# Performance work log

Measured on AMD Instinct MI355X. Metric: run time of the kernel, lower is better.

## Reference

```python
import jax, jax.numpy as jnp
import numpy as np

K = 3  # Chebyshev filter size (max_view)


def avwgcn(X, E, weights_pool, bias_pool):
    """Adaptive node-wise graph conv. X: [B,N,C_in], E: [N,D]."""
    N = E.shape[0]
    # adaptive adjacency: softmax over rows of relu(E E^T)
    supports = jax.nn.softmax(jax.nn.relu(E @ E.T), axis=1)  # [N,N]
    support_set = [jnp.eye(N, dtype=X.dtype), supports]
    for _ in range(2, K):  # Chebyshev recursion
        support_set.append(2.0 * supports @ support_set[-1] - support_set[-2])
    S = jnp.stack(support_set, axis=0)  # [K,N,N]
    W = jnp.einsum('nd,dkio->nkio', E, weights_pool)  # per-node weights [N,K,Ci,Co]
    bias = E @ bias_pool  # [N,Co]
    XG = jnp.einsum('knm,bmc->bnkc', S, X)  # [B,N,K,Ci]
    return jnp.einsum('bnki,nkio->bno', XG, W) + bias  # [B,N,Co]


def setup_inputs() -> dict:
    key = jax.random.key(0)
    ks = jax.random.split(key, 5)
    B, N, Cin, Cout, D = 32, 4096, 2, 64, 10
    Ci = Cin + Cout  # 66
    X = jax.random.normal(ks[0], (B, N, Cin), dtype=jnp.float32)
    H = jnp.zeros((B, N, Cout), dtype=jnp.float32)
    E = jax.random.normal(ks[1], (N, D), dtype=jnp.float32)
    W_gate = jax.random.normal(ks[2], (D, K, Ci, 2 * Cout), dtype=jnp.float32) * 0.1
    b_gate = jnp.zeros((D, 2 * Cout), dtype=jnp.float32)
    W_update = jax.random.normal(ks[3], (D, K, Ci, Cout), dtype=jnp.float32) * 0.1
    b_update = jnp.zeros((D, Cout), dtype=jnp.float32)
    return {"X": X, "H": H, "E": E, "W_gate": W_gate, "b_gate": b_gate,
            "W_update": W_update, "b_update": b_update}


def reference(X, H, E, W_gate, b_gate, W_update, b_update):
    Cout = H.shape[-1]
    XH = jnp.concatenate([X, H], axis=-1)  # [B,N,Cin+Cout]
    ZR = jax.nn.sigmoid(avwgcn(XH, E, W_gate, b_gate))  # [B,N,2*Cout]
    Z, R = ZR[..., :Cout], ZR[..., Cout:]
    C = jnp.concatenate([X, Z * H], axis=-1)
    HC = jnp.tanh(avwgcn(C, E, W_update, b_update))
    return R * H + (1.0 - R) * HC
```

## Files before the change

kernel.cpp:

```cpp
#include <hip/hip_runtime.h>
#include <math.h>

#define N_NODES 4096
#define BATCH   32
#define D_EMB   10
#define CIN     2
#define COUT    64
#define CI      66
#define KSUP    3
#define NCOLS   2112
#define NPAD    2176
#define LDT     4096

#define KSEC    72
#define KI_REAL 216
#define KILD    232
#define OCH     (32 * KILD)
#define WROW_G  (128 * KILD)
#define WROW_U  (64 * KILD)
#define WGT2_R  (WROW_G + WROW_U)

typedef _Float16 half_t;
typedef __attribute__((ext_vector_type(8))) _Float16 f16x8;
typedef __attribute__((ext_vector_type(4))) _Float16 f16x4;
typedef __attribute__((ext_vector_type(2))) _Float16 f16x2;
typedef __attribute__((ext_vector_type(4))) float f32x4;

union u32h2 { unsigned u; f16x2 h; };

struct __attribute__((packed, aligned(4))) uint4_u4 { uint4 v; };
__device__ __forceinline__ f16x8 loadu8h(const half_t* p) {
  union { uint4 u; f16x8 h; } r;
  r.u = ((const uint4_u4*)p)->v;
  return r.h;
}

__device__ __forceinline__ float fast_sigmoid(float x) { return 1.f / (1.f + __expf(-x)); }
__device__ __forceinline__ float fast_tanh(float x) { return 1.f - 2.f / (__expf(2.f * x) + 1.f); }

__device__ __forceinline__ void gld_lds16(const half_t* g, half_t* l) {
  __builtin_amdgcn_global_load_lds(
      (const __attribute__((address_space(1))) void*)g,
      (__attribute__((address_space(3))) void*)l, 16, 0, 0);
}

__global__ __launch_bounds__(256) void k_softmax_p(const float* __restrict__ E,
                                                   half_t* __restrict__ Pb) {
  const int n = blockIdx.x;
  const int tid = threadIdx.x;
  __shared__ float En[D_EMB];
  __shared__ float ms[256], ss[256];
  if (tid < D_EMB) En[tid] = E[n * D_EMB + tid];
  __syncthreads();
  float en[D_EMB];
#pragma unroll
  for (int d = 0; d < D_EMB; ++d) en[d] = En[d];

  float val[16];
  float m = -1e30f, s = 0.f;
#pragma unroll
  for (int it = 0; it < 16; ++it) {
    const int c = tid + it * 256;
    const float* Ec = E + c * D_EMB;
    float v = 0.f;
#pragma unroll
    for (int d = 0; d < D_EMB; ++d) v += en[d] * Ec[d];
    v = fmaxf(v, 0.f);
    val[it] = v;
    if (v > m) { s *= __expf(m - v); m = v; }
    s += __expf(v - m);
  }
  ms[tid] = m; ss[tid] = s;
  __syncthreads();
  for (int off = 128; off > 0; off >>= 1) {
    if (tid < off) {
      float m2 = ms[tid + off], s2 = ss[tid + off];
      float m1 = ms[tid], s1 = ss[tid];
      float mm = fmaxf(m1, m2);
      ms[tid] = mm;
      ss[tid] = s1 * __expf(m1 - mm) + s2 * __expf(m2 - mm);
    }
    __syncthreads();
  }
  const float M = ms[0];
  const float inv = 1.f / ss[0];
  half_t* Pr = Pb + (size_t)n * N_NODES;
#pragma unroll
  for (int it = 0; it < 16; ++it)
    Pr[tid + it * 256] = (half_t)(__expf(val[it] - M) * inv);
}

__global__ __launch_bounds__(256) void k_build_v0(const float* __restrict__ X,
                                                  const float* __restrict__ H,
                                                  half_t* __restrict__ Vt,
                                                  half_t* __restrict__ Vn,
                                                  half_t* __restrict__ Cbn) {
  size_t idx = (size_t)blockIdx.x * 256 + threadIdx.x;
  if (idx >= (size_t)N_NODES * NCOLS) return;
  const int m = (int)(idx / NCOLS);
  const int col = (int)(idx % NCOLS);
  const int b = col / CI;
  const int c = col % CI;
  float v;
  if (c < CIN) v = X[((size_t)b * N_NODES + m) * CIN + c];
  else         v = H[((size_t)b * N_NODES + m) * COUT + (c - CIN)];
  const half_t h = (half_t)v;
  Vn[(size_t)m * NPAD + col] = h;
  Vt[(size_t)col * LDT + m] = h;
  if (c < CIN) Cbn[(size_t)m * NPAD + col] = h;
}

__device__ __forceinline__ void gemm_compute_tile(const half_t* __restrict__ Lb,
                                                  int wm, int wn, int fofs,
                                                  f32x4 (&acc)[4][4]) {
  const half_t* As_ = Lb;
  const half_t* Bs_ = Lb + 4096;
  f16x8 a[4], b[4];
#pragma unroll
  for (int i = 0; i < 4; ++i)
    a[i] = *(const f16x8*)&As_[((wm >> 4) + i) * 512 + fofs];
#pragma unroll
  for (int j = 0; j < 4; ++j)
    b[j] = *(const f16x8*)&Bs_[((wn >> 4) + j) * 512 + fofs];
  __builtin_amdgcn_s_setprio(1);
#pragma unroll
  for (int i = 0; i < 4; ++i)
#pragma unroll
    for (int j = 0; j < 4; ++j)
      acc[i][j] = __builtin_amdgcn_mfma_f32_16x16x32_f16(a[i], b[j], acc[i][j], 0, 0, 0);
  __builtin_amdgcn_s_setprio(0);
}

__global__ __launch_bounds__(256) void k_gemm_f16(const half_t* __restrict__ A,
                                                  const half_t* __restrict__ Bt,
                                                  half_t* __restrict__ Cn,
                                                  half_t* __restrict__ Ct) {
  __shared__ half_t LB[4][8192];
  const int tid = threadIdx.x;
  const int lane = tid & 63;
  const int wave = tid >> 6;

  int flat = blockIdx.y * 17 + blockIdx.x;
  flat = (flat & 7) * 68 + (flat >> 3);
  const int bx = flat % 17;
  const int by = flat / 17;

  const int wm = (wave >> 1) * 64;
  const int wn = (wave & 1) * 64;
  const int rb = by * 128;
  const int cb = bx * 128;

  const int srow = lane >> 2;
  const int skg = (((lane & 3) + ((lane >> 3) & 3)) & 3) * 8;
  const half_t* ga0 = A + (size_t)(rb + wave * 32 + srow) * N_NODES + skg;
  const half_t* ga1 = ga0 + (size_t)16 * N_NODES;
  const half_t* gb0 = Bt + (size_t)(cb + wave * 32 + srow) * LDT + skg;
  const half_t* gb1 = gb0 + (size_t)16 * LDT;
  const int lA0 = wave * 1024;
  const int lA1 = lA0 + 512;
  const int lB0 = 4096 + wave * 1024;
  const int lB1 = lB0 + 512;

  const int fr = lane & 15;
  const int fg = lane >> 4;
  const int fofs = (4 * fr + ((fg - (fr >> 1)) & 3)) * 8;

  f32x4 acc[4][4] = {};

#define STAGE_T(buf, kk) do { half_t* Lp = LB[(buf)]; \
    gld_lds16(ga0 + (kk), Lp + lA0); gld_lds16(ga1 + (kk), Lp + lA1); \
    gld_lds16(gb0 + (kk), Lp + lB0); gld_lds16(gb1 + (kk), Lp + lB1); } while (0)

  STAGE_T(0, 0);
  STAGE_T(1, 32);
  STAGE_T(2, 64);

  for (int t = 0; t < 124; t += 4) {
    asm volatile("s_waitcnt vmcnt(8)\n\ts_barrier" ::: "memory");
    STAGE_T(3, (t + 3) * 32);
    gemm_compute_tile(LB[0], wm, wn, fofs, acc);

    asm volatile("s_waitcnt vmcnt(8)\n\ts_barrier" ::: "memory");
    STAGE_T(0, (t + 4) * 32);
    gemm_compute_tile(LB[1], wm, wn, fofs, acc);

    asm volatile("s_waitcnt vmcnt(8)\n\ts_barrier" ::: "memory");
    STAGE_T(1, (t + 5) * 32);
    gemm_compute_tile(LB[2], wm, wn, fofs, acc);

    asm volatile("s_waitcnt vmcnt(8)\n\ts_barrier" ::: "memory");
    STAGE_T(2, (t + 6) * 32);
    gemm_compute_tile(LB[3], wm, wn, fofs, acc);
  }
  asm volatile("s_waitcnt vmcnt(8)\n\ts_barrier" ::: "memory");
  STAGE_T(3, 127 * 32);
  gemm_compute_tile(LB[0], wm, wn, fofs, acc);
  asm volatile("s_waitcnt vmcnt(8)\n\ts_barrier" ::: "memory");
  gemm_compute_tile(LB[1], wm, wn, fofs, acc);
  asm volatile("s_waitcnt vmcnt(4)\n\ts_barrier" ::: "memory");
  gemm_compute_tile(LB[2], wm, wn, fofs, acc);
  asm volatile("s_waitcnt vmcnt(0)\n\ts_barrier" ::: "memory");
  gemm_compute_tile(LB[3], wm, wn, fofs, acc);
#undef STAGE_T

  const int en = lane & 15;
  const int em = (lane >> 4) * 4;
#pragma unroll
  for (int i = 0; i < 4; ++i) {
#pragma unroll
    for (int j = 0; j < 4; ++j) {
      const int m0 = rb + wm + i * 16 + em;
      const int n = cb + wn + j * 16 + en;
      half_t h0 = (half_t)acc[i][j][0];
      half_t h1 = (half_t)acc[i][j][1];
      half_t h2 = (half_t)acc[i][j][2];
      half_t h3 = (half_t)acc[i][j][3];
      if (Ct) {
        f16x4 t4 = {h0, h1, h2, h3};
        *(f16x4*)&Ct[(size_t)n * LDT + m0] = t4;
      }
      Cn[(size_t)(m0 + 0) * NPAD + n] = h0;
      Cn[(size_t)(m0 + 1) * NPAD + n] = h1;
      Cn[(size_t)(m0 + 2) * NPAD + n] = h2;
      Cn[(size_t)(m0 + 3) * NPAD + n] = h3;
    }
  }
}

__global__ __launch_bounds__(256) void k_tr(const half_t* __restrict__ Cbn,
                                            half_t* __restrict__ Ct) {
  __shared__ half_t T[64][69];
  const int tid = threadIdx.x;
  const int cb = blockIdx.x * 64;
  const int mb = blockIdx.y * 64;
  const int c4 = (tid & 15) * 4;
  const int r0 = tid >> 4;
#pragma unroll
  for (int it = 0; it < 4; ++it) {
    const int r = r0 + it * 16;
    f16x4 v = *(const f16x4*)&Cbn[(size_t)(mb + r) * NPAD + cb + c4];
    T[r][c4 + 0] = v[0];
    T[r][c4 + 1] = v[1];
    T[r][c4 + 2] = v[2];
    T[r][c4 + 3] = v[3];
  }
  __syncthreads();
#pragma unroll
  for (int it = 0; it < 4; ++it) {
    const int c2 = r0 + it * 16;
    const int m4 = c4;
    f16x4 v = {T[m4 + 0][c2], T[m4 + 1][c2], T[m4 + 2][c2], T[m4 + 3][c2]};
    *(f16x4*)&Ct[(size_t)(cb + c2) * LDT + mb + m4] = v;
  }
}

__global__ __launch_bounds__(256) void k_wgt2(const float* __restrict__ Wg,
                                              const float* __restrict__ Wu,
                                              unsigned* __restrict__ WT2) {
  const int r = blockIdx.x * 256 + threadIdx.x;
  if (r >= WGT2_R) return;
  const float* pool;
  int o, ki, ostr;
  if (r < WROW_G) { o = r / KILD; ki = r % KILD; pool = Wg; ostr = 128; }
  else { int r2 = r - WROW_G; o = r2 / KILD; ki = r2 % KILD; pool = Wu; ostr = 64; }
  const int k = ki / KSEC;
  const int i = ki - k * KSEC;
#pragma unroll
  for (int dp = 0; dp < 5; ++dp) {
    u32h2 v; v.h = f16x2{(half_t)0.f, (half_t)0.f};
    if (ki < KI_REAL && i < CI) {
      v.h[0] = (half_t)pool[(((size_t)(2 * dp) * KSUP + k) * CI + i) * ostr + o];
      v.h[1] = (half_t)pool[(((size_t)(2 * dp + 1) * KSUP + k) * CI + i) * ostr + o];
    }
    WT2[(size_t)dp * WGT2_R + r] = v.u;
  }
}

__device__ __forceinline__ void stage_xg(const half_t* __restrict__ v0r,
                                         const half_t* __restrict__ g1r,
                                         const half_t* __restrict__ g2r,
                                         half_t* __restrict__ xg, int tid, int nthr) {
  for (int w = tid; w < 32 * 9; w += nthr) {
    const int b = w / 9;
    const int oct = w - b * 9;
    half_t* row = xg + b * KILD;
    const half_t* pv = v0r + b * CI;
    const half_t* pg1 = g1r + b * CI;
    const half_t* pg2 = g2r + b * CI;
    if (oct < 8) {
      const f16x8 v0 = loadu8h(pv + oct * 8);
      const f16x8 g1 = loadu8h(pg1 + oct * 8);
      const f16x8 g2 = loadu8h(pg2 + oct * 8);
      const f16x8 x2 = g2 + g2 - v0;
      *(f16x8*)&row[oct * 8] = v0;
      *(f16x8*)&row[KSEC + oct * 8] = g1;
      *(f16x8*)&row[2 * KSEC + oct * 8] = x2;
    } else {
      u32h2 tv, tg1, tg2;
      tv.u = *(const unsigned*)(pv + 64);
      tg1.u = *(const unsigned*)(pg1 + 64);
      tg2.u = *(const unsigned*)(pg2 + 64);
      f16x8 v0 = {}, g1 = {}, x2 = {};
      v0[0] = tv.h[0]; v0[1] = tv.h[1];
      g1[0] = tg1.h[0]; g1[1] = tg1.h[1];
      x2[0] = tg2.h[0] + tg2.h[0] - tv.h[0];
      x2[1] = tg2.h[1] + tg2.h[1] - tv.h[1];
      *(f16x8*)&row[64] = v0;
      *(f16x8*)&row[KSEC + 64] = g1;
      *(f16x8*)&row[2 * KSEC + 64] = x2;
    }
  }
  for (int w = tid; w < 32 * 2; w += nthr) {
    const f16x8 z = {};
    *(f16x8*)&xg[(w >> 1) * KILD + KI_REAL + (w & 1) * 8] = z;
  }
}

__global__ __launch_bounds__(512) void k_gate_t(const half_t* __restrict__ Vn,
                                                const half_t* __restrict__ G1n,
                                                const half_t* __restrict__ G2n,
                                                const unsigned* __restrict__ WT2,
                                                const float* __restrict__ E,
                                                const float* __restrict__ bg,
                                                const float* __restrict__ H,
                                                half_t* __restrict__ Cbn,
                                                half_t* __restrict__ Rb) {
  const int n0 = blockIdx.x * 2;
  const int tid = threadIdx.x;
  const int lane = tid & 63;
  const int wave = tid >> 6;
  __shared__ half_t Wl[2][OCH];
  __shared__ half_t xg[2][OCH];
  __shared__ float biasl[2][128];

  f16x2 e2p0[5], e2p1[5];
#pragma unroll
  for (int dp = 0; dp < 5; ++dp) {
    e2p0[dp][0] = (half_t)E[n0 * D_EMB + 2 * dp];
    e2p0[dp][1] = (half_t)E[n0 * D_EMB + 2 * dp + 1];
    e2p1[dp][0] = (half_t)E[(n0 + 1) * D_EMB + 2 * dp];
    e2p1[dp][1] = (half_t)E[(n0 + 1) * D_EMB + 2 * dp + 1];
  }

  if (tid < 256) {
    const int nn = tid >> 7;
    const int o = tid & 127;
    float s = 0.f;
#pragma unroll
    for (int d = 0; d < D_EMB; ++d) s += E[(n0 + nn) * D_EMB + d] * bg[d * 128 + o];
    biasl[nn][o] = s;
  }
  stage_xg(Vn + (size_t)n0 * NPAD, G1n + (size_t)n0 * NPAD, G2n + (size_t)n0 * NPAD, xg[0], tid, 512);
  stage_xg(Vn + (size_t)(n0 + 1) * NPAD, G1n + (size_t)(n0 + 1) * NPAD, G2n + (size_t)(n0 + 1) * NPAD, xg[1], tid, 512);

  const int fr = lane & 15;
  const int fk = (lane >> 4) * 8;
  const int en = lane & 15;
  const int em = (lane >> 4) * 4;
  const int node = wave & 1;
  const int ot = (wave >> 1) & 1;
  const int bh = wave >> 2;
  const int nn = n0 + node;

#pragma unroll
  for (int p = 0; p < 4; ++p) {
    if (p > 0) __syncthreads();
    for (int base = tid * 8; base < OCH; base += 4096) {
      float a0[8] = {}, a1[8] = {};
#pragma unroll
      for (int dp = 0; dp < 5; ++dp) {
        const unsigned* wrow = WT2 + (size_t)dp * WGT2_R + p * OCH + base;
        uint4 wa = *(const uint4*)wrow;
        uint4 wb = *(const uint4*)(wrow + 4);
        u32h2 c0, c1, c2, c3;
        c0.u = wa.x; c1.u = wa.y; c2.u = wa.z; c3.u = wa.w;
        a0[0] = __builtin_amdgcn_fdot2(c0.h, e2p0[dp], a0[0], false);
        a0[1] = __builtin_amdgcn_fdot2(c1.h, e2p0[dp], a0[1], false);
        a0[2] = __builtin_amdgcn_fdot2(c2.h, e2p0[dp], a0[2], false);
        a0[3] = __builtin_amdgcn_fdot2(c3.h, e2p0[dp], a0[3], false);
        a1[0] = __builtin_amdgcn_fdot2(c0.h, e2p1[dp], a1[0], false);
        a1[1] = __builtin_amdgcn_fdot2(c1.h, e2p1[dp], a1[1], false);
        a1[2] = __builtin_amdgcn_fdot2(c2.h, e2p1[dp], a1[2], false);
        a1[3] = __builtin_amdgcn_fdot2(c3.h, e2p1[dp], a1[3], false);
        c0.u = wb.x; c1.u = wb.y; c2.u = wb.z; c3.u = wb.w;
        a0[4] = __builtin_amdgcn_fdot2(c0.h, e2p0[dp], a0[4], false);
        a0[5] = __builtin_amdgcn_fdot2(c1.h, e2p0[dp], a0[5], false);
        a0[6] = __builtin_amdgcn_fdot2(c2.h, e2p0[dp], a0[6], false);
        a0[7] = __builtin_amdgcn_fdot2(c3.h, e2p0[dp], a0[7], false);
        a1[4] = __builtin_amdgcn_fdot2(c0.h, e2p1[dp], a1[4], false);
        a1[5] = __builtin_amdgcn_fdot2(c1.h, e2p1[dp], a1[5], false);
        a1[6] = __builtin_amdgcn_fdot2(c2.h, e2p1[dp], a1[6], false);
        a1[7] = __builtin_amdgcn_fdot2(c3.h, e2p1[dp], a1[7], false);
      }
      f16x8 w0, w1;
#pragma unroll
      for (int e = 0; e < 8; ++e) { w0[e] = (half_t)a0[e]; w1[e] = (half_t)a1[e]; }
      *(f16x8*)&Wl[0][base] = w0;
      *(f16x8*)&Wl[1][base] = w1;
    }
    __syncthreads();

    f32x4 acc2 = {};
#pragma unroll
    for (int ks = 0; ks < 7; ++ks) {
      const f16x8 a0 = *(const f16x8*)&xg[node][(bh * 16 + fr) * KILD + ks * 32 + fk];
      const f16x8 b0 = *(const f16x8*)&Wl[node][(ot * 16 + fr) * KILD + ks * 32 + fk];
      acc2 = __builtin_amdgcn_mfma_f32_16x16x32_f16(a0, b0, acc2, 0, 0, 0);
    }
    const int o_g = p * 32 + ot * 16 + en;
    const float bo = biasl[node][o_g];
#pragma unroll
    for (int r = 0; r < 4; ++r) {
      const int b = bh * 16 + em + r;
      const float s = fast_sigmoid(acc2[r] + bo);
      if (p < 2) {
        const float hv = H[((size_t)b * N_NODES + nn) * COUT + o_g];
        const half_t z = (half_t)(s * hv);
        Cbn[(size_t)nn * NPAD + b * CI + CIN + o_g] = z;
      } else {
        Rb[(size_t)nn * 2048 + b * COUT + (o_g - 64)] = (half_t)s;
      }
    }
  }
}

__global__ __launch_bounds__(512) void k_update_t(const half_t* __restrict__ Cbn,
                                                  const half_t* __restrict__ G1n,
                                                  const half_t* __restrict__ G2n,
                                                  const unsigned* __restrict__ WT2,
                                                  const float* __restrict__ E,
                                                  const float* __restrict__ bu,
                                                  const float* __restrict__ H,
                                                  const half_t* __restrict__ Rb,
                                                  float* __restrict__ Out) {
  const int n0 = blockIdx.x * 2;
  const int tid = threadIdx.x;
  const int lane = tid & 63;
  const int wave = tid >> 6;
  __shared__ half_t Wl[2][OCH];
  __shared__ half_t xg[2][OCH];
  __shared__ float biasl[2][64];

  f16x2 e2p0[5], e2p1[5];
#pragma unroll
  for (int dp = 0; dp < 5; ++dp) {
    e2p0[dp][0] = (half_t)E[n0 * D_EMB + 2 * dp];
    e2p0[dp][1] = (half_t)E[n0 * D_EMB + 2 * dp + 1];
    e2p1[dp][0] = (half_t)E[(n0 + 1) * D_EMB + 2 * dp];
    e2p1[dp][1] = (half_t)E[(n0 + 1) * D_EMB + 2 * dp + 1];
  }

  if (tid < 128) {
    const int nn = tid >> 6;
    const int o = tid & 63;
    float s = 0.f;
#pragma unroll
    for (int d = 0; d < D_EMB; ++d) s += E[(n0 + nn) * D_EMB + d] * bu[d * COUT + o];
    biasl[nn][o] = s;
  }
  stage_xg(Cbn + (size_t)n0 * NPAD, G1n + (size_t)n0 * NPAD, G2n + (size_t)n0 * NPAD, xg[0], tid, 512);
  stage_xg(Cbn + (size_t)(n0 + 1) * NPAD, G1n + (size_t)(n0 + 1) * NPAD, G2n + (size_t)(n0 + 1) * NPAD, xg[1], tid, 512);

  const int fr = lane & 15;
  const int fk = (lane >> 4) * 8;
  const int en = lane & 15;
  const int em = (lane >> 4) * 4;
  const int node = wave & 1;
  const int ot = (wave >> 1) & 1;
  const int bh = wave >> 2;
  const int nn = n0 + node;

#pragma unroll
  for (int p = 0; p < 2; ++p) {
    if (p > 0) __syncthreads();
    for (int base = tid * 8; base < OCH; base += 4096) {
      float a0[8] = {}, a1[8] = {};
#pragma unroll
      for (int dp = 0; dp < 5; ++dp) {
        const unsigned* wrow = WT2 + (size_t)dp * WGT2_R + WROW_G + p * OCH + base;
        uint4 wa = *(const uint4*)wrow;
        uint4 wb = *(const uint4*)(wrow + 4);
        u32h2 c0, c1, c2, c3;
        c0.u = wa.x; c1.u = wa.y; c2.u = wa.z; c3.u = wa.w;
        a0[0] = __builtin_amdgcn_fdot2(c0.h, e2p0[dp], a0[0], false);
        a0[1] = __builtin_amdgcn_fdot2(c1.h, e2p0[dp], a0[1], false);
        a0[2] = __builtin_amdgcn_fdot2(c2.h, e2p0[dp], a0[2], false);
        a0[3] = __builtin_amdgcn_fdot2(c3.h, e2p0[dp], a0[3], false);
        a1[0] = __builtin_amdgcn_fdot2(c0.h, e2p1[dp], a1[0], false);
        a1[1] = __builtin_amdgcn_fdot2(c1.h, e2p1[dp], a1[1], false);
        a1[2] = __builtin_amdgcn_fdot2(c2.h, e2p1[dp], a1[2], false);
        a1[3] = __builtin_amdgcn_fdot2(c3.h, e2p1[dp], a1[3], false);
        c0.u = wb.x; c1.u = wb.y; c2.u = wb.z; c3.u = wb.w;
        a0[4] = __builtin_amdgcn_fdot2(c0.h, e2p0[dp], a0[4], false);
        a0[5] = __builtin_amdgcn_fdot2(c1.h, e2p0[dp], a0[5], false);
        a0[6] = __builtin_amdgcn_fdot2(c2.h, e2p0[dp], a0[6], false);
        a0[7] = __builtin_amdgcn_fdot2(c3.h, e2p0[dp], a0[7], false);
        a1[4] = __builtin_amdgcn_fdot2(c0.h, e2p1[dp], a1[4], false);
        a1[5] = __builtin_amdgcn_fdot2(c1.h, e2p1[dp], a1[5], false);
        a1[6] = __builtin_amdgcn_fdot2(c2.h, e2p1[dp], a1[6], false);
        a1[7] = __builtin_amdgcn_fdot2(c3.h, e2p1[dp], a1[7], false);
      }
      f16x8 w0, w1;
#pragma unroll
      for (int e = 0; e < 8; ++e) { w0[e] = (half_t)a0[e]; w1[e] = (half_t)a1[e]; }
      *(f16x8*)&Wl[0][base] = w0;
      *(f16x8*)&Wl[1][base] = w1;
    }
    __syncthreads();

    f32x4 acc2 = {};
#pragma unroll
    for (int ks = 0; ks < 7; ++ks) {
      const f16x8 a0 = *(const f16x8*)&xg[node][(bh * 16 + fr) * KILD + ks * 32 + fk];
      const f16x8 b0 = *(const f16x8*)&Wl[node][(ot * 16 + fr) * KILD + ks * 32 + fk];
      acc2 = __builtin_amdgcn_mfma_f32_16x16x32_f16(a0, b0, acc2, 0, 0, 0);
    }
    const int o = p * 32 + ot * 16 + en;
    const float bo = biasl[node][o];
#pragma unroll
    for (int r = 0; r < 4; ++r) {
      const int b = bh * 16 + em + r;
      const float hc = fast_tanh(acc2[r] + bo);
      const float hv = H[((size_t)b * N_NODES + nn) * COUT + o];
      const float rr = (float)Rb[(size_t)nn * 2048 + b * COUT + o];
      Out[((size_t)b * N_NODES + nn) * COUT + o] = rr * hv + (1.f - rr) * hc;
    }
  }
}

extern "C" void kernel_launch(void* const* d_in, const int* in_sizes, int n_in,
                              void* d_out, int out_size, void* d_ws, size_t ws_size,
                              hipStream_t stream) {
  const float* X  = (const float*)d_in[0];
  const float* H  = (const float*)d_in[1];
  const float* E  = (const float*)d_in[2];
  const float* Wg = (const float*)d_in[3];
  const float* bg = (const float*)d_in[4];
  const float* Wu = (const float*)d_in[5];
  const float* bu = (const float*)d_in[6];
  float* out = (float*)d_out;

  const size_t SZ_P = (size_t)N_NODES * N_NODES;
  const size_t SZ_M = (size_t)NPAD * LDT;
  half_t* Pb  = (half_t*)d_ws;
  half_t* Vt  = Pb + SZ_P;
  half_t* Vn  = Vt + SZ_M;
  half_t* G1t = Vn + SZ_M;
  half_t* G1n = G1t + SZ_M;
  half_t* G2n = G1n + SZ_M;
  half_t* Cbt = G2n + SZ_M;
  half_t* Cbn = Cbt + SZ_M;
  half_t* Rb  = Cbn + SZ_M;
  unsigned* WT2 = (unsigned*)(Rb + (size_t)BATCH * N_NODES * COUT);

  const dim3 gg(17, 32);
  const dim3 gt(33, 64);

  k_softmax_p<<<N_NODES, 256, 0, stream>>>(E, Pb);
  {
    const size_t tot = (size_t)N_NODES * NCOLS;
    k_build_v0<<<(int)((tot + 255) / 256), 256, 0, stream>>>(X, H, Vt, Vn, Cbn);
  }
  k_wgt2<<<(WGT2_R + 255) / 256, 256, 0, stream>>>(Wg, Wu, WT2);

  k_gemm_f16<<<gg, 256, 0, stream>>>(Pb, Vt, G1n, G1t);
  k_gemm_f16<<<gg, 256, 0, stream>>>(Pb, G1t, G2n, nullptr);
  k_gate_t<<<N_NODES / 2, 512, 0, stream>>>(Vn, G1n, G2n, WT2, E, bg, H, Cbn, Rb);
  k_tr<<<gt, 256, 0, stream>>>(Cbn, Cbt);

  k_gemm_f16<<<gg, 256, 0, stream>>>(Pb, Cbt, G1n, G1t);
  k_gemm_f16<<<gg, 256, 0, stream>>>(Pb, G1t, G2n, nullptr);
  k_update_t<<<N_NODES / 2, 512, 0, stream>>>(Cbn, G1n, G2n, WT2, E, bu, H, Rb, out);
}
```

Measured before the change: 728.3 us.

## Process four nodes per block in gate/update kernels, reusing weight loads and shared buffers

The gate and update kernels now handle four nodes per block instead of two. Each global load of the weight pool rows then feeds fdot2 accumulation for four nodes, which halves total weight-pool traffic. Each wave keeps its XG A-fragments in registers so one shared buffer can be reused for the generated weights, and each wave computes both 16-column output tiles. The cost is more registers (a[4][8] accumulators, af[7] fragments) and half as many blocks, which may lower occupancy and parallelism.

```diff
diff --git a/kernel.cpp b/kernel.cpp
--- a/kernel.cpp
+++ b/kernel.cpp
@@ -276,17 +276,21 @@
   }
 }
 
-__device__ __forceinline__ void stage_xg(const half_t* __restrict__ v0r,
-                                         const half_t* __restrict__ g1r,
-                                         const half_t* __restrict__ g2r,
-                                         half_t* __restrict__ xg, int tid, int nthr) {
-  for (int w = tid; w < 32 * 9; w += nthr) {
-    const int b = w / 9;
-    const int oct = w - b * 9;
-    half_t* row = xg + b * KILD;
-    const half_t* pv = v0r + b * CI;
-    const half_t* pg1 = g1r + b * CI;
-    const half_t* pg2 = g2r + b * CI;
+__device__ __forceinline__ void stage_xg4(const half_t* __restrict__ v0b,
+                                          const half_t* __restrict__ g1b,
+                                          const half_t* __restrict__ g2b,
+                                          half_t* __restrict__ xg,
+                                          int n0, int tid, int nthr) {
+  for (int w = tid; w < 4 * 288; w += nthr) {
+    const int nd = w / 288;
+    const int rem = w - nd * 288;
+    const int b = rem / 9;
+    const int oct = rem - b * 9;
+    const size_t src = (size_t)(n0 + nd) * NPAD + b * CI;
+    half_t* row = xg + nd * OCH + b * KILD;
+    const half_t* pv = v0b + src;
+    const half_t* pg1 = g1b + src;
+    const half_t* pg2 = g2b + src;
     if (oct < 8) {
       const f16x8 v0 = loadu8h(pv + oct * 8);
       const f16x8 g1 = loadu8h(pg1 + oct * 8);
@@ -310,9 +314,11 @@
       *(f16x8*)&row[2 * KSEC + 64] = x2;
     }
   }
-  for (int w = tid; w < 32 * 2; w += nthr) {
-    const f16x8 z = {};
-    *(f16x8*)&xg[(w >> 1) * KILD + KI_REAL + (w & 1) * 8] = z;
+  for (int w = tid; w < 4 * 64; w += nthr) {
+    const int nd = w >> 6;
+    const int z = w & 63;
+    const f16x8 zz = {};
+    *(f16x8*)&xg[nd * OCH + (z >> 1) * KILD + KI_REAL + (z & 1) * 8] = zz;
   }
 }
 
@@ -325,24 +331,23 @@
                                                 const float* __restrict__ H,
                                                 half_t* __restrict__ Cbn,
                                                 half_t* __restrict__ Rb) {
-  const int n0 = blockIdx.x * 2;
+  const int n0 = blockIdx.x * 4;
   const int tid = threadIdx.x;
   const int lane = tid & 63;
   const int wave = tid >> 6;
-  __shared__ half_t Wl[2][OCH];
-  __shared__ half_t xg[2][OCH];
-  __shared__ float biasl[2][128];
-
-  f16x2 e2p0[5], e2p1[5];
-#pragma unroll
-  for (int dp = 0; dp < 5; ++dp) {
-    e2p0[dp][0] = (half_t)E[n0 * D_EMB + 2 * dp];
-    e2p0[dp][1] = (half_t)E[n0 * D_EMB + 2 * dp + 1];
-    e2p1[dp][0] = (half_t)E[(n0 + 1) * D_EMB + 2 * dp];
-    e2p1[dp][1] = (half_t)E[(n0 + 1) * D_EMB + 2 * dp + 1];
-  }
-
-  if (tid < 256) {
+  __shared__ half_t S[4 * OCH];
+  __shared__ float biasl[4][128];
+
+  f16x2 e2p[4][5];
+#pragma unroll
+  for (int nd = 0; nd < 4; ++nd)
+#pragma unroll
+    for (int dp = 0; dp < 5; ++dp) {
+      e2p[nd][dp][0] = (half_t)E[(n0 + nd) * D_EMB + 2 * dp];
+      e2p[nd][dp][1] = (half_t)E[(n0 + nd) * D_EMB + 2 * dp + 1];
+    }
+
+  {
     const int nn = tid >> 7;
     const int o = tid & 127;
     float s = 0.f;
@@ -350,23 +355,28 @@
     for (int d = 0; d < D_EMB; ++d) s += E[(n0 + nn) * D_EMB + d] * bg[d * 128 + o];
     biasl[nn][o] = s;
   }
-  stage_xg(Vn + (size_t)n0 * NPAD, G1n + (size_t)n0 * NPAD, G2n + (size_t)n0 * NPAD, xg[0], tid, 512);
-  stage_xg(Vn + (size_t)(n0 + 1) * NPAD, G1n + (size_t)(n0 + 1) * NPAD, G2n + (size_t)(n0 + 1) * NPAD, xg[1], tid, 512);
+  stage_xg4(Vn, G1n, G2n, S, n0, tid, 512);
+  __syncthreads();
 
   const int fr = lane & 15;
   const int fk = (lane >> 4) * 8;
   const int en = lane & 15;
   const int em = (lane >> 4) * 4;
-  const int node = wave & 1;
-  const int ot = (wave >> 1) & 1;
+  const int node = wave & 3;
   const int bh = wave >> 2;
   const int nn = n0 + node;
+
+  f16x8 af[7];
+#pragma unroll
+  for (int ks = 0; ks < 7; ++ks)
+    af[ks] = *(const f16x8*)&S[node * OCH + (bh * 16 + fr) * KILD + ks * 32 + fk];
+  __syncthreads();
 
 #pragma unroll
   for (int p = 0; p < 4; ++p) {
     if (p > 0) __syncthreads();
     for (int base = tid * 8; base < OCH; base += 4096) {
-      float a0[8] = {}, a1[8] = {};
+      float a[4][8] = {};
 #pragma unroll
       for (int dp = 0; dp < 5; ++dp) {
         const unsigned* wrow = WT2 + (size_t)dp * WGT2_R + p * OCH + base;
@@ -374,51 +384,56 @@
         uint4 wb = *(const uint4*)(wrow + 4);
         u32h2 c0, c1, c2, c3;
         c0.u = wa.x; c1.u = wa.y; c2.u = wa.z; c3.u = wa.w;
-        a0[0] = __builtin_amdgcn_fdot2(c0.h, e2p0[dp], a0[0], false);
-        a0[1] = __builtin_amdgcn_fdot2(c1.h, e2p0[dp], a0[1], false);
-        a0[2] = __builtin_amdgcn_fdot2(c2.h, e2p0[dp], a0[2], false);
-        a0[3] = __builtin_amdgcn_fdot2(c3.h, e2p0[dp], a0[3], false);
-        a1[0] = __builtin_amdgcn_fdot2(c0.h, e2p1[dp], a1[0], false);
-        a1[1] = __builtin_amdgcn_fdot2(c1.h, e2p1[dp], a1[1], false);
-        a1[2] = __builtin_amdgcn_fdot2(c2.h, e2p1[dp], a1[2], false);
-        a1[3] = __builtin_amdgcn_fdot2(c3.h, e2p1[dp], a1[3], false);
+#pragma unroll
+        for (int nd = 0; nd < 4; ++nd) {
+          a[nd][0] = __builtin_amdgcn_fdot2(c0.h, e2p[nd][dp], a[nd][0], false);
+          a[nd][1] = __builtin_amdgcn_fdot2(c1.h, e2p[nd][dp], a[nd][1], false);
+          a[nd][2] = __builtin_amdgcn_fdot2(c2.h, e2p[nd][dp], a[nd][2], false);
+          a[nd][3] = __builtin_amdgcn_fdot2(c3.h, e2p[nd][dp], a[nd][3], false);
+        }
         c0.u = wb.x; c1.u = wb.y; c2.u = wb.z; c3.u = wb.w;
-        a0[4] = __builtin_amdgcn_fdot2(c0.h, e2p0[dp], a0[4], false);
-        a0[5] = __builtin_amdgcn_fdot2(c1.h, e2p0[dp], a0[5], false);
-        a0[6] = __builtin_amdgcn_fdot2(c2.h, e2p0[dp], a0[6], false);
-        a0[7] = __builtin_amdgcn_fdot2(c3.h, e2p0[dp], a0[7], false);
-        a1[4] = __builtin_amdgcn_fdot2(c0.h, e2p1[dp], a1[4], false);
-        a1[5] = __builtin_amdgcn_fdot2(c1.h, e2p1[dp], a1[5], false);
-        a1[6] = __builtin_amdgcn_fdot2(c2.h, e2p1[dp], a1[6], false);
-        a1[7] = __builtin_amdgcn_fdot2(c3.h, e2p1[dp], a1[7], false);
-      }
-      f16x8 w0, w1;
-#pragma unroll
-      for (int e = 0; e < 8; ++e) { w0[e] = (half_t)a0[e]; w1[e] = (half_t)a1[e]; }
-      *(f16x8*)&Wl[0][base] = w0;
-      *(f16x8*)&Wl[1][base] = w1;
+#pragma unroll
+        for (int nd = 0; nd < 4; ++nd) {
+          a[nd][4] = __builtin_amdgcn_fdot2(c0.h, e2p[nd][dp], a[nd][4], false);
+          a[nd][5] = __builtin_amdgcn_fdot2(c1.h, e2p[nd][dp], a[nd][5], false);
+          a[nd][6] = __builtin_amdgcn_fdot2(c2.h, e2p[nd][dp], a[nd][6], false);
+          a[nd][7] = __builtin_amdgcn_fdot2(c3.h, e2p[nd][dp], a[nd][7], false);
+        }
+      }
+#pragma unroll
+      for (int nd = 0; nd < 4; ++nd) {
+        f16x8 w0;
+#pragma unroll
+        for (int e = 0; e < 8; ++e) w0[e] = (half_t)a[nd][e];
+        *(f16x8*)&S[nd * OCH + base] = w0;
+      }
     }
     __syncthreads();
 
-    f32x4 acc2 = {};
+    f32x4 acc2[2] = {};
 #pragma unroll
     for (int ks = 0; ks < 7; ++ks) {
-      const f16x8 a0 = *(const f16x8*)&xg[node][(bh * 16 + fr) * KILD + ks * 32 + fk];
-      const f16x8 b0 = *(const f16x8*)&Wl[node][(ot * 16 + fr) * KILD + ks * 32 + fk];
-      acc2 = __builtin_amdgcn_mfma_f32_16x16x32_f16(a0, b0, acc2, 0, 0, 0);
-    }
-    const int o_g = p * 32 + ot * 16 + en;
-    const float bo = biasl[node][o_g];
-#pragma unroll
-    for (int r = 0; r < 4; ++r) {
-      const int b = bh * 16 + em + r;
-      const float s = fast_sigmoid(acc2[r] + bo);
-      if (p < 2) {
-        const float hv = H[((size_t)b * N_NODES + nn) * COUT + o_g];
-        const half_t z = (half_t)(s * hv);
-        Cbn[(size_t)nn * NPAD + b * CI + CIN + o_g] = z;
-      } else {
-        Rb[(size_t)nn * 2048 + b * COUT + (o_g - 64)] = (half_t)s;
+#pragma unroll
+      for (int ot = 0; ot < 2; ++ot) {
+        const f16x8 b0 = *(const f16x8*)&S[node * OCH + (ot * 16 + fr) * KILD + ks * 32 + fk];
+        acc2[ot] = __builtin_amdgcn_mfma_f32_16x16x32_f16(af[ks], b0, acc2[ot], 0, 0, 0);
+      }
+    }
+#pragma unroll
+    for (int ot = 0; ot < 2; ++ot) {
+      const int o_g = p * 32 + ot * 16 + en;
+      const float bo = biasl[node][o_g];
+#pragma unroll
+      for (int r = 0; r < 4; ++r) {
+        const int b = bh * 16 + em + r;
+        const float s = fast_sigmoid(acc2[ot][r] + bo);
+        if (p < 2) {
+          const float hv = H[((size_t)b * N_NODES + nn) * COUT + o_g];
+          const half_t z = (half_t)(s * hv);
+          Cbn[(size_t)nn * NPAD + b * CI + CIN + o_g] = z;
+        } else {
+          Rb[(size_t)nn * 2048 + b * COUT + (o_g - 64)] = (half_t)s;
+        }
       }
     }
   }
@@ -433,24 +448,23 @@
                                                   const float* __restrict__ H,
                                                   const half_t* __restrict__ Rb,
                                                   float* __restrict__ Out) {
-  const int n0 = blockIdx.x * 2;
+  const int n0 = blockIdx.x * 4;
   const int tid = threadIdx.x;
   const int lane = tid & 63;
   const int wave = tid >> 6;
-  __shared__ half_t Wl[2][OCH];
-  __shared__ half_t xg[2][OCH];
-  __shared__ float biasl[2][64];
-
-  f16x2 e2p0[5], e2p1[5];
-#pragma unroll
-  for (int dp = 0; dp < 5; ++dp) {
-    e2p0[dp][0] = (half_t)E[n0 * D_EMB + 2 * dp];
-    e2p0[dp][1] = (half_t)E[n0 * D_EMB + 2 * dp + 1];
-    e2p1[dp][0] = (half_t)E[(n0 + 1) * D_EMB + 2 * dp];
-    e2p1[dp][1] = (half_t)E[(n0 + 1) * D_EMB + 2 * dp + 1];
-  }
-
-  if (tid < 128) {
+  __shared__ half_t S[4 * OCH];
+  __shared__ float biasl[4][64];
+
+  f16x2 e2p[4][5];
+#pragma unroll
+  for (int nd = 0; nd < 4; ++nd)
+#pragma unroll
+    for (int dp = 0; dp < 5; ++dp) {
+      e2p[nd][dp][0] = (half_t)E[(n0 + nd) * D_EMB + 2 * dp];
+      e2p[nd][dp][1] = (half_t)E[(n0 + nd) * D_EMB + 2 * dp + 1];
+    }
+
+  if (tid < 256) {
     const int nn = tid >> 6;
     const int o = tid & 63;
     float s = 0.f;
@@ -458,23 +472,28 @@
     for (int d = 0; d < D_EMB; ++d) s += E[(n0 + nn) * D_EMB + d] * bu[d * COUT + o];
     biasl[nn][o] = s;
   }
-  stage_xg(Cbn + (size_t)n0 * NPAD, G1n + (size_t)n0 * NPAD, G2n + (size_t)n0 * NPAD, xg[0], tid, 512);
-  stage_xg(Cbn + (size_t)(n0 + 1) * NPAD, G1n + (size_t)(n0 + 1) * NPAD, G2n + (size_t)(n0 + 1) * NPAD, xg[1], tid, 512);
+  stage_xg4(Cbn, G1n, G2n, S, n0, tid, 512);
+  __syncthreads();
 
   const int fr = lane & 15;
   const int fk = (lane >> 4) * 8;
   const int en = lane & 15;
   const int em = (lane >> 4) * 4;
-  const int node = wave & 1;
-  const int ot = (wave >> 1) & 1;
+  const int node = wave & 3;
   const int bh = wave >> 2;
   const int nn = n0 + node;
+
+  f16x8 af[7];
+#pragma unroll
+  for (int ks = 0; ks < 7; ++ks)
+    af[ks] = *(const f16x8*)&S[node * OCH + (bh * 16 + fr) * KILD + ks * 32 + fk];
+  __syncthreads();
 
 #pragma unroll
   for (int p = 0; p < 2; ++p) {
     if (p > 0) __syncthreads();
     for (int base = tid * 8; base < OCH; base += 4096) {
-      float a0[8] = {}, a1[8] = {};
+      float a[4][8] = {};
 #pragma unroll
       for (int dp = 0; dp < 5; ++dp) {
         const unsigned* wrow = WT2 + (size_t)dp * WGT2_R + WROW_G + p * OCH + base;
@@ -482,48 +501,53 @@
         uint4 wb = *(const uint4*)(wrow + 4);
         u32h2 c0, c1, c2, c3;
         c0.u = wa.x; c1.u = wa.y; c2.u = wa.z; c3.u = wa.w;
-        a0[0] = __builtin_amdgcn_fdot2(c0.h, e2p0[dp], a0[0], false);
-        a0[1] = __builtin_amdgcn_fdot2(c1.h, e2p0[dp], a0[1], false);
-        a0[2] = __builtin_amdgcn_fdot2(c2.h, e2p0[dp], a0[2], false);
-        a0[3] = __builtin_amdgcn_fdot2(c3.h, e2p0[dp], a0[3], false);
-        a1[0] = __builtin_amdgcn_fdot2(c0.h, e2p1[dp], a1[0], false);
-        a1[1] = __builtin_amdgcn_fdot2(c1.h, e2p1[dp], a1[1], false);
-        a1[2] = __builtin_amdgcn_fdot2(c2.h, e2p1[dp], a1[2], false);
-        a1[3] = __builtin_amdgcn_fdot2(c3.h, e2p1[dp], a1[3], false);
+#pragma unroll
+        for (int nd = 0; nd < 4; ++nd) {
+          a[nd][0] = __builtin_amdgcn_fdot2(c0.h, e2p[nd][dp], a[nd][0], false);
+          a[nd][1] = __builtin_amdgcn_fdot2(c1.h, e2p[nd][dp], a[nd][1], false);
+          a[nd][2] = __builtin_amdgcn_fdot2(c2.h, e2p[nd][dp], a[nd][2], false);
+          a[nd][3] = __builtin_amdgcn_fdot2(c3.h, e2p[nd][dp], a[nd][3], false);
+        }
         c0.u = wb.x; c1.u = wb.y; c2.u = wb.z; c3.u = wb.w;
-        a0[4] = __builtin_amdgcn_fdot2(c0.h, e2p0[dp], a0[4], false);
-        a0[5] = __builtin_amdgcn_fdot2(c1.h, e2p0[dp], a0[5], false);
-        a0[6] = __builtin_amdgcn_fdot2(c2.h, e2p0[dp], a0[6], false);
-        a0[7] = __builtin_amdgcn_fdot2(c3.h, e2p0[dp], a0[7], false);
-        a1[4] = __builtin_amdgcn_fdot2(c0.h, e2p1[dp], a1[4], false);
-        a1[5] = __builtin_amdgcn_fdot2(c1.h, e2p1[dp], a1[5], false);
-        a1[6] = __builtin_amdgcn_fdot2(c2.h, e2p1[dp], a1[6], false);
-        a1[7] = __builtin_amdgcn_fdot2(c3.h, e2p1[dp], a1[7], false);
-      }
-      f16x8 w0, w1;
-#pragma unroll
-      for (int e = 0; e < 8; ++e) { w0[e] = (half_t)a0[e]; w1[e] = (half_t)a1[e]; }
-      *(f16x8*)&Wl[0][base] = w0;
-      *(f16x8*)&Wl[1][base] = w1;
+#pragma unroll
+        for (int nd = 0; nd < 4; ++nd) {
+          a[nd][4] = __builtin_amdgcn_fdot2(c0.h, e2p[nd][dp], a[nd][4], false);
+          a[nd][5] = __builtin_amdgcn_fdot2(c1.h, e2p[nd][dp], a[nd][5], false);
+          a[nd][6] = __builtin_amdgcn_fdot2(c2.h, e2p[nd][dp], a[nd][6], false);
+          a[nd][7] = __builtin_amdgcn_fdot2(c3.h, e2p[nd][dp], a[nd][7], false);
+        }
+      }
+#pragma unroll
+      for (int nd = 0; nd < 4; ++nd) {
+        f16x8 w0;
+#pragma unroll
+        for (int e = 0; e < 8; ++e) w0[e] = (half_t)a[nd][e];
+        *(f16x8*)&S[nd * OCH + base] = w0;
+      }
     }
     __syncthreads();
 
-    f32x4 acc2 = {};
+    f32x4 acc2[2] = {};
 #pragma unroll
     for (int ks = 0; ks < 7; ++ks) {
-      const f16x8 a0 = *(const f16x8*)&xg[node][(bh * 16 + fr) * KILD + ks * 32 + fk];
-      const f16x8 b0 = *(const f16x8*)&Wl[node][(ot * 16 + fr) * KILD + ks * 32 + fk];
-      acc2 = __builtin_amdgcn_mfma_f32_16x16x32_f16(a0, b0, acc2, 0, 0, 0);
-    }
-    const int o = p * 32 + ot * 16 + en;
-    const float bo = biasl[node][o];
-#pragma unroll
-    for (int r = 0; r < 4; ++r) {
-      const int b = bh * 16 + em + r;
-      const float hc = fast_tanh(acc2[r] + bo);
-      const float hv = H[((size_t)b * N_NODES + nn) * COUT + o];
-      const float rr = (float)Rb[(size_t)nn * 2048 + b * COUT + o];
-      Out[((size_t)b * N_NODES + nn) * COUT + o] = rr * hv + (1.f - rr) * hc;
+#pragma unroll
+      for (int ot = 0; ot < 2; ++ot) {
+        const f16x8 b0 = *(const f16x8*)&S[node * OCH + (ot * 16 + fr) * KILD + ks * 32 + fk];
+        acc2[ot] = __builtin_amdgcn_mfma_f32_16x16x32_f16(af[ks], b0, acc2[ot], 0, 0, 0);
+      }
+    }
+#pragma unroll
+    for (int ot = 0; ot < 2; ++ot) {
+      const int o = p * 32 + ot * 16 + en;
+      const float bo = biasl[node][o];
+#pragma unroll
+      for (int r = 0; r < 4; ++r) {
+        const int b = bh * 16 + em + r;
+        const float hc = fast_tanh(acc2[ot][r] + bo);
+        const float hv = H[((size_t)b * N_NODES + nn) * COUT + o];
+        const float rr = (float)Rb[(size_t)nn * 2048 + b * COUT + o];
+        Out[((size_t)b * N_NODES + nn) * COUT + o] = rr * hv + (1.f - rr) * hc;
+      }
     }
   }
 }
@@ -565,10 +589,10 @@
 
   k_gemm_f16<<<gg, 256, 0, stream>>>(Pb, Vt, G1n, G1t);
   k_gemm_f16<<<gg, 256, 0, stream>>>(Pb, G1t, G2n, nullptr);
-  k_gate_t<<<N_NODES / 2, 512, 0, stream>>>(Vn, G1n, G2n, WT2, E, bg, H, Cbn, Rb);
+  k_gate_t<<<N_NODES / 4, 512, 0, stream>>>(Vn, G1n, G2n, WT2, E, bg, H, Cbn, Rb);
   k_tr<<<gt, 256, 0, stream>>>(Cbn, Cbt);
 
   k_gemm_f16<<<gg, 256, 0, stream>>>(Pb, Cbt, G1n, G1t);
   k_gemm_f16<<<gg, 256, 0, stream>>>(Pb, G1t, G2n, nullptr);
-  k_update_t<<<N_NODES / 2, 512, 0, stream>>>(Cbn, G1n, G2n, WT2, E, bu, H, Rb, out);
-}
+  k_update_t<<<N_NODES / 4, 512, 0, stream>>>(Cbn, G1n, G2n, WT2, E, bu, H, Rb, out);
+}
```

New measurement: 716.1 us. No clear change (-1.7%).
